# Kernel optimization log

Measured on AMD Instinct MI355X. Metric: run time of the kernel, lower is better.

Reference implementation:

```python
import jax, jax.numpy as jnp
import numpy as np

N_NODES, N_EDGES = 50000, 150000
HEADS, OUT = 2, 325


def _lin(k, i, o):
    return (jax.random.normal(k, (i, o), jnp.float32) / np.float32(np.sqrt(i)))


def setup_inputs() -> dict:
    key = jax.random.key(0)
    ks = jax.random.split(key, 24)
    h = jax.random.normal(ks[0], (N_NODES, 5), jnp.float32)
    edge_num = jax.random.normal(ks[1], (N_NODES, 5), jnp.float32)
    edge_index = jax.random.randint(ks[2], (2, N_EDGES), 0, N_NODES)
    edge_weight = jax.random.uniform(ks[3], (N_EDGES,), jnp.float32)
    d = dict(h=h, edge_num=edge_num, edge_index=edge_index, edge_weight=edge_weight)
    # five GCNConv layers: weight [5,64], bias [64]
    names = ['sum', 'mean', 'max', 'ne', 'nem']
    for i, nm in enumerate(names):
        d['W_' + nm] = _lin(ks[4 + i], 5, 64)
        d['b_' + nm] = jnp.zeros((64,), jnp.float32)
    # GATv2Conv params
    d['Wl'] = _lin(ks[10], 325, HEADS * OUT)
    d['Wr'] = _lin(ks[11], 325, HEADS * OUT)
    d['We'] = _lin(ks[12], 1, HEADS * OUT)
    d['att'] = jax.random.normal(ks[13], (HEADS, OUT), jnp.float32) / np.float32(np.sqrt(OUT))
    d['b_att'] = jnp.zeros((OUT,), jnp.float32)
    d['W_fc1'] = _lin(ks[14], 325, 5)
    d['b_fc1'] = jnp.zeros((5,), jnp.float32)
    return d


def _seg_mean(m, idx, n):
    s = jax.ops.segment_sum(m, idx, n)
    c = jax.ops.segment_sum(jnp.ones((m.shape[0],), m.dtype), idx, n)
    return s / jnp.clip(c, 1.0)[:, None]


def _seg_max0(m, idx, n):
    o = jax.ops.segment_max(m, idx, n)
    return jnp.where(jnp.isfinite(o), o, jnp.zeros_like(o))  # empty segments -> 0 (PyG behavior)


def _gcn(x, W, b, src, dst, w, aggr, n):
    # GCNConv(normalize=False, add_self_loops=False): aggr_j w_ij * (x_j @ W) + b
    m = (x @ W)[src]
    if w is not None:
        m = m * w[:, None]
    if aggr == 'add':
        o = jax.ops.segment_sum(m, dst, n)
    elif aggr == 'mean':
        o = _seg_mean(m, dst, n)
    else:
        o = _seg_max0(m, dst, n)
    return o + b


def _forward(h, edge_num, edge_weight, W_sum, b_sum, W_mean, b_mean, W_max, b_max,
             W_ne, b_ne, W_nem, b_nem, Wl, Wr, We, att, b_att, W_fc1, b_fc1, edge_index):
    n = h.shape[0]
    src, dst = edge_index[0], edge_index[1]
    h1 = _gcn(h, W_sum, b_sum, src, dst, edge_weight, 'add', n)
    h2 = _gcn(h, W_mean, b_mean, src, dst, edge_weight, 'mean', n)
    h3 = _gcn(h, W_max, b_max, src, dst, edge_weight, 'max', n)
    h4 = _gcn(h, W_ne, b_ne, src, dst, None, 'add', n)
    h5 = _gcn(h, W_nem, b_nem, src, dst, None, 'max', n)
    x = jnp.concatenate([h1, h2, h3, h4, h5, edge_num], axis=-1)  # [N, 325]
    # GATv2Conv(heads=2, concat=False, aggr='mean', add_self_loops=True, fill_value='mean')
    loop = jnp.arange(n)
    src2 = jnp.concatenate([src, loop])
    dst2 = jnp.concatenate([dst, loop])
    ea = jnp.concatenate([edge_weight[:, None], jnp.full((n, 1), jnp.mean(edge_weight))], axis=0)
    xl = (x @ Wl).reshape(n, HEADS, OUT)  # source transform
    xr = (x @ Wr).reshape(n, HEADS, OUT)  # target transform
    ee = (ea @ We).reshape(-1, HEADS, OUT)
    f = jax.nn.leaky_relu(xl[src2] + xr[dst2] + ee, 0.2)  # [E2, H, C]
    alpha = jnp.einsum('ehc,hc->eh', f, att)
    mx = jax.ops.segment_max(alpha, dst2, n)
    a = jnp.exp(alpha - mx[dst2])
    a = a / jax.ops.segment_sum(a, dst2, n)[dst2]  # softmax over incoming edges
    msg = xl[src2] * a[:, :, None]
    cnt = jax.ops.segment_sum(jnp.ones((src2.shape[0],), x.dtype), dst2, n)
    agg = jax.ops.segment_sum(msg, dst2, n) / jnp.clip(cnt, 1.0)[:, None, None]  # aggr='mean'
    o = agg.mean(axis=1) + b_att  # concat=False -> head mean
    return o @ W_fc1 + b_fc1


def reference(h, edge_num, edge_index, edge_weight, W_sum, b_sum, W_mean, b_mean,
              W_max, b_max, W_ne, b_ne, W_nem, b_nem, Wl, Wr, We, att, b_att,
              W_fc1, b_fc1):
    return _forward(h, edge_num, edge_weight, W_sum, b_sum, W_mean, b_mean, W_max, b_max,
                    W_ne, b_ne, W_nem, b_nem, Wl, Wr, We, att, b_att, W_fc1, b_fc1, edge_index)
```

## Files before the change

### kernel.cpp

```cpp
#include <hip/hip_runtime.h>
#include <hip/hip_bf16.h>
#include <math.h>

#define N_NODES 50000
#define N_EDGES 150000
#define FDIM 325
#define KP 352
#define HCP 1312
#define XROFF 656
#define LDA 40
#define LDC 136
#define NPAN 391
#define NBJ 11
#define SCAN_B 256
#define NBLK ((N_NODES + SCAN_B - 1) / SCAN_B)

typedef unsigned short ushort_t;
typedef __attribute__((ext_vector_type(8))) short short8v;
typedef __attribute__((ext_vector_type(4))) float f32x4;

__device__ __forceinline__ float bf2f(ushort_t u) {
  return __uint_as_float(((unsigned)u) << 16);
}
__device__ __forceinline__ ushort_t f2bf(float f) {
  __hip_bfloat16 h = __float2bfloat16(f);
  union { __hip_bfloat16 h; ushort_t u; } cv; cv.h = h;
  return cv.u;
}

__global__ void k_init(int* deg, int* cursor, float* red) {
  int i = blockIdx.x * blockDim.x + threadIdx.x;
  if (i < N_NODES) { deg[i] = 0; cursor[i] = 0; }
  if (i == 0) red[0] = 0.f;
}

__global__ void k_count(const int* __restrict__ dst, const float* __restrict__ ew,
                        int* deg, float* red) {
  int e = blockIdx.x * blockDim.x + threadIdx.x;
  float w = 0.f;
  if (e < N_EDGES) { atomicAdd(&deg[dst[e]], 1); w = ew[e]; }
  #pragma unroll
  for (int m = 32; m; m >>= 1) w += __shfl_xor(w, m);
  if ((threadIdx.x & 63) == 0) atomicAdd(red, w);
}

__global__ void k_scan1(const int* __restrict__ deg, int* offs, int* bsum) {
  __shared__ int buf[SCAN_B];
  int b = blockIdx.x, tid = threadIdx.x, i = b * SCAN_B + tid;
  int v = (i < N_NODES) ? deg[i] : 0;
  buf[tid] = v;
  __syncthreads();
  for (int o = 1; o < SCAN_B; o <<= 1) {
    int t = (tid >= o) ? buf[tid - o] : 0;
    __syncthreads();
    buf[tid] += t;
    __syncthreads();
  }
  if (i < N_NODES) offs[i + 1] = buf[tid];
  if (tid == SCAN_B - 1) bsum[b] = buf[tid];
}
__global__ void k_scan2(const int* __restrict__ bsum, int* bofs) {
  __shared__ int buf[256];
  int tid = threadIdx.x;
  int v = (tid < NBLK) ? bsum[tid] : 0;
  buf[tid] = v;
  __syncthreads();
  for (int o = 1; o < 256; o <<= 1) {
    int t = (tid >= o) ? buf[tid - o] : 0;
    __syncthreads();
    buf[tid] += t;
    __syncthreads();
  }
  if (tid < NBLK) bofs[tid] = buf[tid] - v;
}
__global__ void k_scan3(const int* __restrict__ bofs, int* offs) {
  int i = blockIdx.x * blockDim.x + threadIdx.x;
  if (i == 0) offs[0] = 0;
  if (i < N_NODES) offs[i + 1] += bofs[i / SCAN_B];
}

__global__ void k_scatter(const int* __restrict__ src, const int* __restrict__ dst,
                          const float* __restrict__ ew, const int* __restrict__ offs,
                          int* cursor, int* csr_src, float* csr_w) {
  int e = blockIdx.x * blockDim.x + threadIdx.x;
  if (e >= N_EDGES) return;
  int d = dst[e];
  int p = offs[d] + atomicAdd(&cursor[d], 1);
  csr_src[p] = src[e];
  csr_w[p] = ew[e];
}

__global__ void __launch_bounds__(64) k_gcn(
    const float* __restrict__ h, const float* __restrict__ edge_num,
    const int* __restrict__ offs, const int* __restrict__ csr_src,
    const float* __restrict__ csr_w,
    const float* __restrict__ Wsum, const float* __restrict__ bsum,
    const float* __restrict__ Wmean, const float* __restrict__ bmean,
    const float* __restrict__ Wmax, const float* __restrict__ bmax,
    const float* __restrict__ Wne, const float* __restrict__ bne,
    const float* __restrict__ Wnem, const float* __restrict__ bnem,
    ushort_t* __restrict__ x) {
  int n = blockIdx.x;
  int t = threadIdx.x;
  float w0[5], w1[5], w2[5], w3[5], w4[5];
  #pragma unroll
  for (int k = 0; k < 5; ++k) {
    w0[k] = Wsum[k * 64 + t];
    w1[k] = Wmean[k * 64 + t];
    w2[k] = Wmax[k * 64 + t];
    w3[k] = Wne[k * 64 + t];
    w4[k] = Wnem[k * 64 + t];
  }
  float s_sum = 0.f, s_wmean = 0.f, s_max = -INFINITY, s_ne = 0.f, s_nem = -INFINITY;
  int beg = offs[n], end = offs[n + 1];
  float wcur = 0.f, hcur[5];
  if (beg < end) {
    int s = csr_src[beg];
    wcur = csr_w[beg];
    #pragma unroll
    for (int k = 0; k < 5; ++k) hcur[k] = h[s * 5 + k];
  }
  for (int i = beg; i < end; ++i) {
    float wnxt = 0.f, hnxt[5];
    if (i + 1 < end) {
      int s = csr_src[i + 1];
      wnxt = csr_w[i + 1];
      #pragma unroll
      for (int k = 0; k < 5; ++k) hnxt[k] = h[s * 5 + k];
    }
    float v0 = 0, v1 = 0, v2 = 0, v3 = 0, v4 = 0;
    #pragma unroll
    for (int k = 0; k < 5; ++k) {
      v0 += hcur[k] * w0[k]; v1 += hcur[k] * w1[k]; v2 += hcur[k] * w2[k];
      v3 += hcur[k] * w3[k]; v4 += hcur[k] * w4[k];
    }
    s_sum += wcur * v0;
    s_wmean += wcur * v1;
    s_max = fmaxf(s_max, wcur * v2);
    s_ne += v3;
    s_nem = fmaxf(s_nem, v4);
    wcur = wnxt;
    #pragma unroll
    for (int k = 0; k < 5; ++k) hcur[k] = hnxt[k];
  }
  int dg = end - beg;
  float inv = 1.f / (float)(dg > 0 ? dg : 1);
  ushort_t* xr = x + (size_t)n * KP;
  xr[t]       = f2bf(s_sum + bsum[t]);
  xr[64 + t]  = f2bf(s_wmean * inv + bmean[t]);
  xr[128 + t] = f2bf((dg ? s_max : 0.f) + bmax[t]);
  xr[192 + t] = f2bf(s_ne + bne[t]);
  xr[256 + t] = f2bf((dg ? s_nem : 0.f) + bnem[t]);
  if (t < 5) xr[320 + t] = f2bf(edge_num[n * 5 + t]);
  if (t < KP - FDIM) xr[FDIM + t] = 0;
}

__global__ void k_wt(const float* __restrict__ Wl, const float* __restrict__ Wr,
                     ushort_t* __restrict__ Wt) {
  int t = blockIdx.x * blockDim.x + threadIdx.x;
  if (t >= HCP * KP) return;
  int n = t / KP, k = t % KP;
  float v = 0.f;
  if (k < FDIM) {
    if (n < 650) v = Wl[(size_t)k * 650 + n];
    else if (n >= XROFF && n < XROFF + 650) v = Wr[(size_t)k * 650 + (n - XROFF)];
  }
  Wt[t] = f2bf(v);
}

__global__ void __launch_bounds__(256) k_gemm_mfma(
    const ushort_t* __restrict__ x, const ushort_t* __restrict__ Wt,
    ushort_t* __restrict__ xlr) {
  __shared__ ushort_t smem[128 * LDA * 2];
  ushort_t* As = smem;
  ushort_t* Bs = smem + 128 * LDA;
  ushort_t* Cs = smem;

  int L = blockIdx.x;
  int panel, jb;
  if (L < 4224) {
    int chunk = L / 88, g = L % 88;
    panel = chunk * 8 + (g & 7);
    jb = g >> 3;
  } else {
    int g = L - 4224;
    panel = 384 + g % 7;
    jb = g / 7;
  }
  int bm = panel * 128, bn = jb * 128;

  int tid = threadIdx.x;
  int lane = tid & 63, wave = tid >> 6;
  int wr = wave >> 1, wc = wave & 1;
  f32x4 acc[4][4] = {};
  for (int k0 = 0; k0 < KP; k0 += 32) {
    #pragma unroll
    for (int it = 0; it < 2; ++it) {
      int idx = tid + it * 256;
      int row = idx >> 2, kc = (idx & 3) << 3;
      int gm = bm + row;
      float4 av = make_float4(0.f, 0.f, 0.f, 0.f);
      if (gm < N_NODES) av = *(const float4*)&x[(size_t)gm * KP + k0 + kc];
      *(float4*)&As[row * LDA + kc] = av;
      int gn = bn + row;
      float4 bv = make_float4(0.f, 0.f, 0.f, 0.f);
      if (gn < HCP) bv = *(const float4*)&Wt[(size_t)gn * KP + k0 + kc];
      *(float4*)&Bs[row * LDA + kc] = bv;
    }
    __syncthreads();
    int koff = (lane >> 4) << 3;
    int ar = (wr << 6) + (lane & 15);
    int br = (wc << 6) + (lane & 15);
    short8v a[4], b[4];
    #pragma unroll
    for (int i = 0; i < 4; ++i) a[i] = *(const short8v*)&As[(ar + i * 16) * LDA + koff];
    #pragma unroll
    for (int j = 0; j < 4; ++j) b[j] = *(const short8v*)&Bs[(br + j * 16) * LDA + koff];
    #pragma unroll
    for (int i = 0; i < 4; ++i)
      #pragma unroll
      for (int j = 0; j < 4; ++j)
        acc[i][j] = __builtin_amdgcn_mfma_f32_16x16x32_bf16(a[i], b[j], acc[i][j], 0, 0, 0);
    __syncthreads();
  }
  #pragma unroll
  for (int half = 0; half < 2; ++half) {
    if (wr == half) {
      int lr0 = ((lane >> 4) << 2);
      int c0 = (wc << 6) + (lane & 15);
      #pragma unroll
      for (int i = 0; i < 4; ++i)
        #pragma unroll
        for (int j = 0; j < 4; ++j)
          #pragma unroll
          for (int r = 0; r < 4; ++r)
            Cs[(lr0 + i * 16 + r) * LDC + c0 + j * 16] = f2bf(acc[i][j][r]);
    }
    __syncthreads();
    #pragma unroll
    for (int it = 0; it < 4; ++it) {
      int idx = tid + it * 256;
      int lr = idx >> 4, cc = idx & 15;
      int row = bm + half * 64 + lr;
      int col = bn + cc * 8;
      if (row < N_NODES && col < HCP) {
        short8v v = *(const short8v*)&Cs[lr * LDC + cc * 8];
        *(short8v*)&xlr[(size_t)row * HCP + col] = v;
      }
    }
    __syncthreads();
  }
}

__global__ void k_wlf(const float* __restrict__ Wl, const float* __restrict__ Wfc,
                      float* __restrict__ Wlf) {
  int t = blockIdx.x * blockDim.x + threadIdx.x;
  if (t >= FDIM * 10) return;
  int cp = t / 10, o = t % 10;
  int hh = o / 5, j = o % 5;
  float s = 0.f;
  for (int c = 0; c < 325; ++c) s += Wl[(size_t)cp * 650 + hh * 325 + c] * Wfc[c * 5 + j];
  Wlf[cp * 10 + o] = s;
}

__global__ void k_yl(const ushort_t* __restrict__ x, const float* __restrict__ Wlf,
                     float* __restrict__ yl) {
  int wid = (blockIdx.x * blockDim.x + threadIdx.x) >> 6;
  int lane = threadIdx.x & 63;
  if (wid >= N_NODES) return;
  const ushort_t* row = x + (size_t)wid * KP;
  float p[10] = {};
  for (int c = lane; c < FDIM; c += 64) {
    float v = bf2f(row[c]);
    const float* wr = Wlf + c * 10;
    #pragma unroll
    for (int j = 0; j < 10; ++j) p[j] += v * wr[j];
  }
  #pragma unroll
  for (int j = 0; j < 10; ++j)
    #pragma unroll
    for (int m = 32; m; m >>= 1) p[j] += __shfl_xor(p[j], m);
  if (lane == 0) {
    #pragma unroll
    for (int j = 0; j < 10; ++j) yl[(size_t)wid * 10 + j] = p[j];
  }
}

__global__ void k_cvec(const float* __restrict__ b_att, const float* __restrict__ Wfc,
                       const float* __restrict__ b_fc1, const float* __restrict__ red,
                       float* __restrict__ cvec) {
  int j = threadIdx.x;
  if (j == 5) cvec[5] = red[0] / (float)N_EDGES;
  if (j < 5) {
    float s = b_fc1[j];
    for (int c = 0; c < 325; ++c) s += b_att[c] * Wfc[c * 5 + j];
    cvec[j] = s;
  }
}

__global__ void __launch_bounds__(256) k_att(
    const int* __restrict__ offs, const int* __restrict__ csrs,
    const float* __restrict__ csrw, const ushort_t* __restrict__ xlr,
    const float* __restrict__ We, const float* __restrict__ att,
    const float* __restrict__ cvec, const float* __restrict__ yl,
    float* __restrict__ out) {
  int d = (blockIdx.x * blockDim.x + threadIdx.x) >> 6;
  int lane = threadIdx.x & 63;
  if (d >= N_NODES) return;
  float xd0[8], xd1[8], We0[8], We1[8], at0[8], at1[8];
  const ushort_t* xd = xlr + (size_t)d * HCP + XROFF;
  {
    short8v v = *(const short8v*)&xd[lane * 8];
    int c0 = lane * 8;
    #pragma unroll
    for (int e = 0; e < 8; ++e) {
      xd0[e] = bf2f((ushort_t)v[e]);
      We0[e] = We[c0 + e];
      at0[e] = att[c0 + e];
    }
  }
  if (lane < 18) {
    short8v v = *(const short8v*)&xd[512 + lane * 8];
    int c0 = 512 + lane * 8;
    #pragma unroll
    for (int e = 0; e < 8; ++e) {
      bool ok = (c0 + e) < 650;
      xd1[e] = bf2f((ushort_t)v[e]);
      We1[e] = ok ? We[c0 + e] : 0.f;
      at1[e] = ok ? att[c0 + e] : 0.f;
    }
  }
  float meanw = cvec[5];
  int beg = offs[d], end = offs[d + 1];
  float m0 = -INFINITY, m1 = -INFINITY, s0 = 0.f, s1 = 0.f;
  float oj = 0.f;

  float ea_c, yv_c = 0.f;
  short8v v0_c, v1_c;
  {
    int s;
    if (beg < end) { s = csrs[beg]; ea_c = csrw[beg]; }
    else { s = d; ea_c = meanw; }
    const ushort_t* xs = xlr + (size_t)s * HCP;
    v0_c = *(const short8v*)&xs[lane * 8];
    if (lane < 18) v1_c = *(const short8v*)&xs[512 + lane * 8];
    if (lane < 10) yv_c = yl[(size_t)s * 10 + lane];
  }
  for (int i = beg; i <= end; ++i) {
    float ea_n = 0.f, yv_n = 0.f;
    short8v v0_n, v1_n;
    bool have_next = (i < end);
    if (have_next) {
      int s;
      if (i + 1 < end) { s = csrs[i + 1]; ea_n = csrw[i + 1]; }
      else { s = d; ea_n = meanw; }
      const ushort_t* xs = xlr + (size_t)s * HCP;
      v0_n = *(const short8v*)&xs[lane * 8];
      if (lane < 18) v1_n = *(const short8v*)&xs[512 + lane * 8];
      if (lane < 10) yv_n = yl[(size_t)s * 10 + lane];
    }
    float p0 = 0.f, p1 = 0.f;
    {
      int c0 = lane * 8;
      #pragma unroll
      for (int e = 0; e < 8; ++e) {
        float vv = bf2f((ushort_t)v0_c[e]) + xd0[e] + ea_c * We0[e];
        vv = (vv > 0.f) ? vv : 0.2f * vv;
        float t = vv * at0[e];
        if (c0 + e < 325) p0 += t; else p1 += t;
      }
    }
    if (lane < 18) {
      #pragma unroll
      for (int e = 0; e < 8; ++e) {
        float vv = bf2f((ushort_t)v1_c[e]) + xd1[e] + ea_c * We1[e];
        vv = (vv > 0.f) ? vv : 0.2f * vv;
        p1 += vv * at1[e];
      }
    }
    #pragma unroll
    for (int m = 32; m; m >>= 1) { p0 += __shfl_xor(p0, m); p1 += __shfl_xor(p1, m); }
    float nm0 = fmaxf(m0, p0), nm1 = fmaxf(m1, p1);
    float r0 = __expf(m0 - nm0), r1 = __expf(m1 - nm1);
    float e0 = __expf(p0 - nm0), e1 = __expf(p1 - nm1);
    s0 = s0 * r0 + e0; s1 = s1 * r1 + e1;
    m0 = nm0; m1 = nm1;
    if (lane < 10) {
      float r = (lane < 5) ? r0 : r1;
      float e = (lane < 5) ? e0 : e1;
      oj = oj * r + e * yv_c;
    }
    if (have_next) { ea_c = ea_n; yv_c = yv_n; v0_c = v0_n; v1_c = v1_n; }
  }
  float on = oj / ((lane < 5) ? s0 : s1);
  float other = __shfl(on, lane + 5);
  if (lane < 5) {
    int dg = end - beg;
    out[(size_t)d * 5 + lane] = (on + other) / (2.f * (float)(dg + 1)) + cvec[lane];
  }
}

extern "C" void kernel_launch(void* const* d_in, const int* in_sizes, int n_in,
                              void* d_out, int out_size, void* d_ws, size_t ws_size,
                              hipStream_t stream) {
  (void)in_sizes; (void)n_in; (void)out_size; (void)ws_size;
  const float* h        = (const float*)d_in[0];
  const float* edge_num = (const float*)d_in[1];
  const int*   eidx     = (const int*)d_in[2];
  const float* ew       = (const float*)d_in[3];
  const float* Wsum  = (const float*)d_in[4];  const float* bsum_  = (const float*)d_in[5];
  const float* Wmean = (const float*)d_in[6];  const float* bmean = (const float*)d_in[7];
  const float* Wmax  = (const float*)d_in[8];  const float* bmax  = (const float*)d_in[9];
  const float* Wne   = (const float*)d_in[10]; const float* bne   = (const float*)d_in[11];
  const float* Wnem  = (const float*)d_in[12]; const float* bnem  = (const float*)d_in[13];
  const float* Wl    = (const float*)d_in[14]; const float* Wr    = (const float*)d_in[15];
  const float* We    = (const float*)d_in[16]; const float* att   = (const float*)d_in[17];
  const float* b_att = (const float*)d_in[18];
  const float* Wfc   = (const float*)d_in[19]; const float* bfc   = (const float*)d_in[20];
  const int* src = eidx;
  const int* dst = eidx + N_EDGES;
  float* out = (float*)d_out;

  char* p = (char*)d_ws;
  size_t off = 0;
  auto alloc = [&](size_t bytes) { char* r = p + off; off = (off + bytes + 255) & ~(size_t)255; return r; };
  ushort_t* x   = (ushort_t*)alloc((size_t)N_NODES * KP * 2);
  ushort_t* xlr = (ushort_t*)alloc((size_t)N_NODES * HCP * 2);
  ushort_t* Wt  = (ushort_t*)alloc((size_t)HCP * KP * 2);
  float* yl     = (float*)alloc((size_t)N_NODES * 10 * 4);
  int*   deg    = (int*)alloc((size_t)N_NODES * 4);
  int*   offs   = (int*)alloc((size_t)(N_NODES + 1) * 4);
  int*   cursor = (int*)alloc((size_t)N_NODES * 4);
  int*   csrs   = (int*)alloc((size_t)N_EDGES * 4);
  float* csrw   = (float*)alloc((size_t)N_EDGES * 4);
  int*   bsum   = (int*)alloc((size_t)NBLK * 4);
  int*   bofs   = (int*)alloc((size_t)NBLK * 4);
  float* Wlf    = (float*)alloc((size_t)FDIM * 10 * 4);
  float* red    = (float*)alloc(64);
  float* cvec   = (float*)alloc(64);

  k_init<<<(N_NODES + 255) / 256, 256, 0, stream>>>(deg, cursor, red);
  k_count<<<(N_EDGES + 255) / 256, 256, 0, stream>>>(dst, ew, deg, red);
  k_scan1<<<NBLK, SCAN_B, 0, stream>>>(deg, offs, bsum);
  k_scan2<<<1, 256, 0, stream>>>(bsum, bofs);
  k_scan3<<<NBLK, SCAN_B, 0, stream>>>(bofs, offs);
  k_scatter<<<(N_EDGES + 255) / 256, 256, 0, stream>>>(src, dst, ew, offs, cursor, csrs, csrw);
  k_gcn<<<N_NODES, 64, 0, stream>>>(h, edge_num, offs, csrs, csrw,
                                    Wsum, bsum_, Wmean, bmean, Wmax, bmax,
                                    Wne, bne, Wnem, bnem, x);
  k_wt<<<(HCP * KP + 255) / 256, 256, 0, stream>>>(Wl, Wr, Wt);
  k_gemm_mfma<<<NPAN * NBJ, 256, 0, stream>>>(x, Wt, xlr);
  k_wlf<<<(FDIM * 10 + 255) / 256, 256, 0, stream>>>(Wl, Wfc, Wlf);
  k_yl<<<(N_NODES * 64 + 255) / 256, 256, 0, stream>>>(x, Wlf, yl);
  k_cvec<<<1, 64, 0, stream>>>(b_att, Wfc, bfc, red, cvec);
  k_att<<<(N_NODES * 64 + 255) / 256, 256, 0, stream>>>(offs, csrs, csrw, xlr,
                                                        We, att, cvec, yl, out);
}
```

Baseline: 464.1 us.

## Prefetch next GEMM K-tile into registers and launch attention one wave per block

The MFMA GEMM now loads the next 32-wide K slice of x and Wt into registers right after the shared-memory barrier, so global loads overlap the MFMA work on the current tile instead of stalling before each barrier. The attention kernel is relaunched with one 64-thread block per destination node, which removes the bounds check and the per-wave index math. Prefetching adds register pressure in the GEMM, and the single-wave blocks raise the block count for the attention pass.

```diff
diff --git a/kernel.cpp b/kernel.cpp
--- a/kernel.cpp
+++ b/kernel.cpp
@@ -192,22 +192,34 @@
   int tid = threadIdx.x;
   int lane = tid & 63, wave = tid >> 6;
   int wr = wave >> 1, wc = wave & 1;
+  int srow = tid >> 2, skc = (tid & 3) << 3;
+  const float4 fz = make_float4(0.f, 0.f, 0.f, 0.f);
+
+  float4 pa0, pa1, pb0, pb1;
+  {
+    int gm0 = bm + srow, gm1 = gm0 + 64;
+    int gn0 = bn + srow, gn1 = gn0 + 64;
+    pa0 = (gm0 < N_NODES) ? *(const float4*)&x[(size_t)gm0 * KP + skc] : fz;
+    pa1 = (gm1 < N_NODES) ? *(const float4*)&x[(size_t)gm1 * KP + skc] : fz;
+    pb0 = (gn0 < HCP)     ? *(const float4*)&Wt[(size_t)gn0 * KP + skc] : fz;
+    pb1 = (gn1 < HCP)     ? *(const float4*)&Wt[(size_t)gn1 * KP + skc] : fz;
+  }
   f32x4 acc[4][4] = {};
   for (int k0 = 0; k0 < KP; k0 += 32) {
-    #pragma unroll
-    for (int it = 0; it < 2; ++it) {
-      int idx = tid + it * 256;
-      int row = idx >> 2, kc = (idx & 3) << 3;
-      int gm = bm + row;
-      float4 av = make_float4(0.f, 0.f, 0.f, 0.f);
-      if (gm < N_NODES) av = *(const float4*)&x[(size_t)gm * KP + k0 + kc];
-      *(float4*)&As[row * LDA + kc] = av;
-      int gn = bn + row;
-      float4 bv = make_float4(0.f, 0.f, 0.f, 0.f);
-      if (gn < HCP) bv = *(const float4*)&Wt[(size_t)gn * KP + k0 + kc];
-      *(float4*)&Bs[row * LDA + kc] = bv;
-    }
-    __syncthreads();
+    *(float4*)&As[srow * LDA + skc]        = pa0;
+    *(float4*)&As[(srow + 64) * LDA + skc] = pa1;
+    *(float4*)&Bs[srow * LDA + skc]        = pb0;
+    *(float4*)&Bs[(srow + 64) * LDA + skc] = pb1;
+    __syncthreads();
+    int kn = k0 + 32;
+    if (kn < KP) {
+      int gm0 = bm + srow, gm1 = gm0 + 64;
+      int gn0 = bn + srow, gn1 = gn0 + 64;
+      pa0 = (gm0 < N_NODES) ? *(const float4*)&x[(size_t)gm0 * KP + kn + skc] : fz;
+      pa1 = (gm1 < N_NODES) ? *(const float4*)&x[(size_t)gm1 * KP + kn + skc] : fz;
+      pb0 = (gn0 < HCP)     ? *(const float4*)&Wt[(size_t)gn0 * KP + kn + skc] : fz;
+      pb1 = (gn1 < HCP)     ? *(const float4*)&Wt[(size_t)gn1 * KP + kn + skc] : fz;
+    }
     int koff = (lane >> 4) << 3;
     int ar = (wr << 6) + (lane & 15);
     int br = (wc << 6) + (lane & 15);
@@ -298,15 +310,14 @@
   }
 }
 
-__global__ void __launch_bounds__(256) k_att(
+__global__ void __launch_bounds__(64) k_att(
     const int* __restrict__ offs, const int* __restrict__ csrs,
     const float* __restrict__ csrw, const ushort_t* __restrict__ xlr,
     const float* __restrict__ We, const float* __restrict__ att,
     const float* __restrict__ cvec, const float* __restrict__ yl,
     float* __restrict__ out) {
-  int d = (blockIdx.x * blockDim.x + threadIdx.x) >> 6;
-  int lane = threadIdx.x & 63;
-  if (d >= N_NODES) return;
+  int d = blockIdx.x;
+  int lane = threadIdx.x;
   float xd0[8], xd1[8], We0[8], We1[8], at0[8], at1[8];
   const ushort_t* xd = xlr + (size_t)d * HCP + XROFF;
   {
@@ -453,6 +464,5 @@
   k_wlf<<<(FDIM * 10 + 255) / 256, 256, 0, stream>>>(Wl, Wfc, Wlf);
   k_yl<<<(N_NODES * 64 + 255) / 256, 256, 0, stream>>>(x, Wlf, yl);
   k_cvec<<<1, 64, 0, stream>>>(b_att, Wfc, bfc, red, cvec);
-  k_att<<<(N_NODES * 64 + 255) / 256, 256, 0, stream>>>(offs, csrs, csrw, xlr,
-                                                        We, att, cvec, yl, out);
-}
+  k_att<<<N_NODES, 64, 0, stream>>>(offs, csrs, csrw, xlr, We, att, cvec, yl, out);
+}
```

New measurement: 410.4 us. -11.6%, faster.
